# Performance work log

Measured on AMD Instinct MI355X. Metric: run time of the kernel, lower is better.

Reference implementation:

```python
import jax, jax.numpy as jnp
import numpy as np

TOP_K = 1000  # init kwarg top_k

def setup_inputs() -> dict:
    key = jax.random.key(0)
    k1, k2 = jax.random.split(key)
    scores = jax.random.uniform(k1, (8, 120000, 80), dtype=jnp.float32)
    boxes = jax.random.normal(k2, (8, 120000, 4), dtype=jnp.float32)
    return {"scores": scores, "boxes": boxes}

def reference(scores, boxes):
    # scores: [B, A, C], boxes: [B, A, 4]  (filter_per_class=True path)
    B, A, C = scores.shape
    K = min(TOP_K, A)
    # per-class top-k over anchors
    s_t = jnp.transpose(scores, (0, 2, 1))            # [B, C, A]
    vals, idx = jax.lax.top_k(s_t, K)                 # [B, C, K]
    vals = jnp.transpose(vals, (0, 2, 1))             # [B, K, C]
    idx = jnp.transpose(idx, (0, 2, 1))               # [B, K, C]
    # gather boxes along anchor dim with batch_dims=1 semantics
    b = jnp.arange(B)[:, None, None]                  # [B,1,1]
    boxes_out = boxes[b, idx]                         # [B, K, C, 4]
    return vals, boxes_out
```

## Files before the change

### kernel.cpp

```cpp
#include <hip/hip_runtime.h>


constexpr int B_ = 8;
constexpr int A_ = 120000;
constexpr int C_ = 80;
constexpr int K_ = 1000;
constexpr int NT = 256;

constexpr int S_ = 240;
constexpr int ROWS = A_ / S_;
constexpr float CUT = 0.98958333f;
constexpr float XSCALE = 1048576.0f;
constexpr int CAP = 2048;
constexpr int PCAP = 16;
constexpr int SORT1 = 1024;
constexpr int SORT2 = 2048;

constexpr size_t GCNT_OFF = 0;
constexpr size_t GCNT_BYTES = (size_t)B_ * C_ * 4;
constexpr size_t GCAND_OFF = 4096;
constexpr size_t GCAND_BYTES = (size_t)B_ * C_ * CAP * 8;
constexpr size_t WS_NEED = GCAND_OFF + GCAND_BYTES;

__device__ __forceinline__ unsigned mono_key(float f) {
    unsigned bits = __float_as_uint(f);
    return (bits & 0x80000000u) ? ~bits : (bits | 0x80000000u);
}
__device__ __forceinline__ int xbin(float v) {
    int x = (int)((v - CUT) * XSCALE);
    return x < 0 ? 0 : (x > 16383 ? 16383 : x);
}

__global__ __launch_bounds__(NT)
void stage_kernel(const float* __restrict__ scores,
                  unsigned* __restrict__ gcount,
                  unsigned long long* __restrict__ gcand) {
    const int b = blockIdx.x / S_;
    const int s = blockIdx.x % S_;
    const int t = threadIdx.x;

    __shared__ unsigned long long st[C_ * PCAP];
    __shared__ unsigned cnt[C_];
    __shared__ unsigned base[C_];

    for (int i = t; i < C_; i += NT) cnt[i] = 0;
    __syncthreads();

    const float4* slab = (const float4*)(scores + ((size_t)b * A_ + (size_t)s * ROWS) * C_);
    constexpr int NVEC = ROWS * C_ / 4;
    int c0 = (4 * t) % C_;
    int a  = s * ROWS + (4 * t) / C_;
    for (int i = t; i < NVEC; i += NT) {
        float4 v = slab[i];
        const float vv[4] = {v.x, v.y, v.z, v.w};
        #pragma unroll
        for (int e = 0; e < 4; ++e) {
            if (vv[e] >= CUT) {
                const unsigned key = __float_as_uint(vv[e]) | 0x80000000u;
                const int c = c0 + e;
                const unsigned slot = atomicAdd(&cnt[c], 1u);
                const unsigned long long pk =
                    ((unsigned long long)key << 32) | (unsigned)(~(unsigned)a);
                if (slot < (unsigned)PCAP) {
                    st[c * PCAP + slot] = pk;
                } else {
                    const int bc = b * C_ + c;
                    const unsigned g = atomicAdd(&gcount[bc], 1u);
                    if (g < (unsigned)CAP) gcand[(size_t)bc * CAP + g] = pk;
                }
            }
        }
        c0 += 64;
        a += 12;
        if (c0 >= C_) { c0 -= C_; a += 1; }
    }
    __syncthreads();

    if (t < C_) {
        const unsigned nc = cnt[t] < (unsigned)PCAP ? cnt[t] : (unsigned)PCAP;
        base[t] = nc ? atomicAdd(&gcount[b * C_ + t], nc) : 0u;
    }
    __syncthreads();

    for (int i = t; i < C_ * PCAP; i += NT) {
        const int c = i / PCAP;
        const unsigned j = (unsigned)(i % PCAP);
        const unsigned nc = cnt[c] < (unsigned)PCAP ? cnt[c] : (unsigned)PCAP;
        if (j < nc) {
            const unsigned pos = base[c] + j;
            if (pos < (unsigned)CAP)
                gcand[((size_t)(b * C_ + c)) * CAP + pos] = st[i];
        }
    }
}

__global__ __launch_bounds__(NT)
void sort_emit_kernel(const float* __restrict__ scores, const float* __restrict__ boxes,
                      const unsigned* __restrict__ gcount,
                      const unsigned long long* __restrict__ gcand,
                      float* __restrict__ out) {
    const int blk = blockIdx.x;
    const int b = blk & 7;
    const int c = blk >> 3;
    const int bc = b * C_ + c;
    const int t = threadIdx.x;

    __shared__ unsigned long long buf[SORT2];
    __shared__ unsigned hist4k[4096];
    __shared__ unsigned coarse[NT];
    __shared__ unsigned s_tb, s_m, s_mhi, s_tb2, s_m2, s_cnt;
    __shared__ unsigned s_boundBin, s_boundCnt, s_aboveAdd;

    const unsigned n = gcount[bc];
    bool fast = (n >= (unsigned)K_ && n <= (unsigned)CAP);
    int ss = SORT1;
    int mode = 0;

    if (fast) {
        const unsigned long long* src = gcand + (size_t)bc * CAP;
        for (int i = t; i < 256; i += NT) hist4k[i] = 0;
        __syncthreads();
        for (unsigned i = t; i < n; i += NT) {
            const unsigned key = (unsigned)(src[i] >> 32);
            const int x = xbin(__uint_as_float(key & 0x7FFFFFFFu));
            atomicAdd(&hist4k[x >> 7], 1u);
        }
        __syncthreads();
        if (t == 0) {
            unsigned run = 0;
            int tb = 0;
            for (int i = 127; i >= 0; --i) {
                run += hist4k[i];
                if (run >= (unsigned)K_) { tb = i; break; }
            }
            s_tb = (unsigned)tb; s_m = run; s_mhi = run - hist4k[tb]; s_cnt = 0;
        }
        __syncthreads();
        const int tb = (int)s_tb;
        const unsigned m = s_m;

        if (m > (unsigned)SORT1) {
            for (unsigned i = t; i < n; i += NT) {
                const unsigned key = (unsigned)(src[i] >> 32);
                const int x = xbin(__uint_as_float(key & 0x7FFFFFFFu));
                if ((x >> 7) == tb) atomicAdd(&hist4k[128 + (x & 127)], 1u);
            }
            __syncthreads();
            if (t == 0) {
                unsigned run = s_mhi;
                int tb2 = 0;
                for (int i = 127; i >= 0; --i) {
                    run += hist4k[128 + i];
                    if (run >= (unsigned)K_) { tb2 = i; break; }
                }
                s_tb2 = (unsigned)tb2; s_m2 = run;
            }
            __syncthreads();
            if (s_m2 <= (unsigned)SORT1)      { mode = 1; ss = SORT1; }
            else if (m <= (unsigned)SORT2)    { mode = 0; ss = SORT2; }
            else                              { fast = false; }
        }

        if (fast) {
            const int tb2 = (int)s_tb2;
            const unsigned mm = (mode == 1) ? s_m2 : s_m;
            for (unsigned i = t; i < n; i += NT) {
                const unsigned long long e = src[i];
                const unsigned key = (unsigned)(e >> 32);
                const int x = xbin(__uint_as_float(key & 0x7FFFFFFFu));
                const int fb = x >> 7;
                bool take = (mode == 0) ? (fb >= tb)
                                        : (fb > tb || (fb == tb && (x & 127) >= tb2));
                if (take) buf[atomicAdd(&s_cnt, 1u)] = e;
            }
            __syncthreads();
            for (int i = (int)mm + t; i < ss; i += NT) buf[i] = 0ull;
            __syncthreads();
        }
    }

    if (!fast) {
        ss = SORT2;
        const float* sc = scores + (size_t)b * A_ * C_ + c;
        unsigned aboveCum = 0, pref = 0, T32 = 0;
        for (int lv = 0; lv < 3; ++lv) {
            const int shift = (lv == 0) ? 20 : (lv == 1) ? 8 : 0;
            const int nb = (lv == 2) ? 256 : 4096;
            for (int i = t; i < nb; i += NT) hist4k[i] = 0;
            __syncthreads();
            for (int a = t; a < A_; a += NT) {
                unsigned key = mono_key(sc[(size_t)a * C_]);
                bool ok = (lv == 0) || (lv == 1 ? ((key >> 20) == pref) : ((key >> 8) == pref));
                if (ok) atomicAdd(&hist4k[(key >> shift) & (nb - 1)], 1u);
            }
            __syncthreads();
            const int chunk = nb / NT;
            {
                unsigned ssum = 0;
                for (int i = 0; i < chunk; ++i) ssum += hist4k[t * chunk + i];
                coarse[t] = ssum;
            }
            __syncthreads();
            if (t == 0) {
                const unsigned target = K_ - aboveCum;
                unsigned run = 0;
                int cb = NT - 1;
                for (; cb > 0; --cb) { if (run + coarse[cb] >= target) break; run += coarse[cb]; }
                int bin = cb * chunk + (chunk - 1);
                for (; bin > cb * chunk; --bin) { if (run + hist4k[bin] >= target) break; run += hist4k[bin]; }
                s_boundBin = (unsigned)bin; s_boundCnt = hist4k[bin]; s_aboveAdd = run;
            }
            __syncthreads();
            const unsigned bin = s_boundBin, bcn = s_boundCnt, addAbove = s_aboveAdd;
            __syncthreads();
            aboveCum += addAbove;
            pref = (lv == 0) ? bin : (lv == 1) ? ((pref << 12) | bin) : ((pref << 8) | bin);
            if (aboveCum + bcn <= (unsigned)SORT2 || lv == 2) {
                T32 = (lv == 0) ? (pref << 20) : (lv == 1) ? (pref << 8) : pref;
                break;
            }
        }
        if (t == 0) s_cnt = 0;
        __syncthreads();
        for (int a = t; a < A_; a += NT) {
            unsigned key = mono_key(sc[(size_t)a * C_]);
            if (key >= T32) {
                unsigned slot = atomicAdd(&s_cnt, 1u);
                if (slot < (unsigned)SORT2)
                    buf[slot] = ((unsigned long long)key << 32) | (unsigned)(~(unsigned)a);
            }
        }
        __syncthreads();
        const unsigned nn = (s_cnt < (unsigned)SORT2) ? s_cnt : (unsigned)SORT2;
        for (int i = (int)nn + t; i < SORT2; i += NT) buf[i] = 0ull;
        __syncthreads();
    }

    for (unsigned kk = 2; kk <= (unsigned)ss; kk <<= 1) {
        for (unsigned j = kk >> 1; j > 0; j >>= 1) {
            __syncthreads();
            for (int i = t; i < ss; i += NT) {
                const int ixj = i ^ (int)j;
                if (ixj > i) {
                    const bool up = ((i & kk) == 0);
                    unsigned long long x = buf[i], y = buf[ixj];
                    if ((x < y) == up) { buf[i] = y; buf[ixj] = x; }
                }
            }
        }
    }
    __syncthreads();

    float* vals_out = out;
    float* boxes_out = out + (size_t)B_ * K_ * C_;
    const float4* bx = (const float4*)(boxes + (size_t)b * A_ * 4);
    for (int kk = t; kk < K_; kk += NT) {
        const unsigned long long e = buf[kk];
        const unsigned key = (unsigned)(e >> 32);
        const unsigned aidx = ~(unsigned)e;
        const unsigned bitsv = (key & 0x80000000u) ? (key ^ 0x80000000u) : ~key;
        vals_out[((size_t)b * K_ + kk) * C_ + c] = __uint_as_float(bitsv);
        const float4 bb = bx[aidx];
        *(float4*)&boxes_out[(((size_t)b * K_ + kk) * C_ + c) * 4] = bb;
    }
}

__global__ __launch_bounds__(NT)
void topk_select_kernel(const float* __restrict__ scores,
                        const float* __restrict__ boxes,
                        float* __restrict__ out) {
    const int blk = blockIdx.x;
    const int b = blk / C_;
    const int c = blk % C_;
    const float* sc = scores + (size_t)b * A_ * C_ + c;
    constexpr int LCAP = 2048;
    __shared__ unsigned hist[4096];
    __shared__ unsigned coarse[NT];
    __shared__ unsigned long long cand[LCAP];
    __shared__ unsigned s_n, s_boundBin, s_boundCnt, s_aboveAdd;
    const int t = threadIdx.x;
    unsigned aboveCum = 0, pref = 0, T32 = 0;
    for (int lv = 0; lv < 3; ++lv) {
        const int shift = (lv == 0) ? 20 : (lv == 1) ? 8 : 0;
        const int nb = (lv == 2) ? 256 : 4096;
        for (int i = t; i < nb; i += NT) hist[i] = 0;
        __syncthreads();
        for (int a = t; a < A_; a += NT) {
            unsigned key = mono_key(sc[(size_t)a * C_]);
            bool ok = (lv == 0) || (lv == 1 ? ((key >> 20) == pref) : ((key >> 8) == pref));
            if (ok) atomicAdd(&hist[(key >> shift) & (nb - 1)], 1u);
        }
        __syncthreads();
        const int chunk = nb / NT;
        {
            unsigned ssum = 0;
            for (int i = 0; i < chunk; ++i) ssum += hist[t * chunk + i];
            coarse[t] = ssum;
        }
        __syncthreads();
        if (t == 0) {
            const unsigned target = K_ - aboveCum;
            unsigned run = 0;
            int cb = NT - 1;
            for (; cb > 0; --cb) { if (run + coarse[cb] >= target) break; run += coarse[cb]; }
            int bin = cb * chunk + (chunk - 1);
            for (; bin > cb * chunk; --bin) { if (run + hist[bin] >= target) break; run += hist[bin]; }
            s_boundBin = (unsigned)bin; s_boundCnt = hist[bin]; s_aboveAdd = run;
        }
        __syncthreads();
        const unsigned bin = s_boundBin, bcn = s_boundCnt, addAbove = s_aboveAdd;
        __syncthreads();
        aboveCum += addAbove;
        pref = (lv == 0) ? bin : (lv == 1) ? ((pref << 12) | bin) : ((pref << 8) | bin);
        if (aboveCum + bcn <= (unsigned)LCAP || lv == 2) {
            T32 = (lv == 0) ? (pref << 20) : (lv == 1) ? (pref << 8) : pref;
            break;
        }
    }
    if (t == 0) s_n = 0;
    __syncthreads();
    for (int a = t; a < A_; a += NT) {
        unsigned key = mono_key(sc[(size_t)a * C_]);
        if (key >= T32) {
            unsigned slot = atomicAdd(&s_n, 1u);
            if (slot < (unsigned)LCAP)
                cand[slot] = ((unsigned long long)key << 32) | (unsigned)(~(unsigned)a);
        }
    }
    __syncthreads();
    const unsigned n = (s_n < (unsigned)LCAP) ? s_n : (unsigned)LCAP;
    for (int i = (int)n + t; i < LCAP; i += NT) cand[i] = 0ull;
    __syncthreads();
    for (unsigned kk = 2; kk <= (unsigned)LCAP; kk <<= 1) {
        for (unsigned j = kk >> 1; j > 0; j >>= 1) {
            __syncthreads();
            for (int i = t; i < LCAP; i += NT) {
                const int ixj = i ^ (int)j;
                if (ixj > i) {
                    const bool up = ((i & kk) == 0);
                    unsigned long long x = cand[i], y = cand[ixj];
                    if ((x < y) == up) { cand[i] = y; cand[ixj] = x; }
                }
            }
        }
    }
    __syncthreads();
    float* vals_out = out;
    float* boxes_out = out + (size_t)B_ * K_ * C_;
    const float4* bx = (const float4*)(boxes + (size_t)b * A_ * 4);
    for (int kk = t; kk < K_; kk += NT) {
        const unsigned long long e = cand[kk];
        const unsigned key = (unsigned)(e >> 32);
        const unsigned aidx = ~(unsigned)e;
        const unsigned bitsv = (key & 0x80000000u) ? (key ^ 0x80000000u) : ~key;
        vals_out[((size_t)b * K_ + kk) * C_ + c] = __uint_as_float(bitsv);
        const float4 bb = bx[aidx];
        *(float4*)&boxes_out[(((size_t)b * K_ + kk) * C_ + c) * 4] = bb;
    }
}

extern "C" void kernel_launch(void* const* d_in, const int* in_sizes, int n_in,
                              void* d_out, int out_size, void* d_ws, size_t ws_size,
                              hipStream_t stream) {
    const float* scores = (const float*)d_in[0];
    const float* boxes  = (const float*)d_in[1];
    float* out = (float*)d_out;

    if (ws_size < WS_NEED) {
        hipLaunchKernelGGL(topk_select_kernel, dim3(B_ * C_), dim3(NT), 0, stream,
                           scores, boxes, out);
        return;
    }

    char* ws = (char*)d_ws;
    unsigned* gcount = (unsigned*)(ws + GCNT_OFF);
    unsigned long long* gcand = (unsigned long long*)(ws + GCAND_OFF);

    hipMemsetAsync(gcount, 0, GCNT_BYTES, stream);
    hipLaunchKernelGGL(stage_kernel, dim3(B_ * S_), dim3(NT), 0, stream,
                       scores, gcount, gcand);
    hipLaunchKernelGGL(sort_emit_kernel, dim3(B_ * C_), dim3(NT), 0, stream,
                       scores, boxes, gcount, gcand, out);
}
```

Before: 124.5 us.

## Double the sort block size, parallelize histogram threshold scans, prefetch stage loads

The sort/emit kernel now runs 512 threads per block instead of 256, so more threads share the bitonic sort and candidate passes. The single-thread serial scans that find the threshold bins are replaced by parallel suffix-sum scans over 128 bins. The stage kernel software-prefetches the next float4 of scores before processing the current one to overlap load latency with compare/atomic work. The gains come at the cost of more barriers in the scan, higher register and LDS pressure, and possibly fewer resident blocks per CU.

```diff
diff --git a/kernel.cpp b/kernel.cpp
--- a/kernel.cpp
+++ b/kernel.cpp
@@ -6,6 +6,7 @@
 constexpr int C_ = 80;
 constexpr int K_ = 1000;
 constexpr int NT = 256;
+constexpr int NT2 = 512;
 
 constexpr int S_ = 240;
 constexpr int ROWS = A_ / S_;
@@ -50,8 +51,13 @@
     constexpr int NVEC = ROWS * C_ / 4;
     int c0 = (4 * t) % C_;
     int a  = s * ROWS + (4 * t) / C_;
-    for (int i = t; i < NVEC; i += NT) {
-        float4 v = slab[i];
+    int i = t;
+    float4 v = make_float4(0.f, 0.f, 0.f, 0.f);
+    if (i < NVEC) v = slab[i];
+    while (i < NVEC) {
+        const int in = i + NT;
+        float4 vn = v;
+        if (in < NVEC) vn = slab[in];
         const float vv[4] = {v.x, v.y, v.z, v.w};
         #pragma unroll
         for (int e = 0; e < 4; ++e) {
@@ -73,6 +79,8 @@
         c0 += 64;
         a += 12;
         if (c0 >= C_) { c0 -= C_; a += 1; }
+        i = in;
+        v = vn;
     }
     __syncthreads();
 
@@ -82,19 +90,19 @@
     }
     __syncthreads();
 
-    for (int i = t; i < C_ * PCAP; i += NT) {
-        const int c = i / PCAP;
-        const unsigned j = (unsigned)(i % PCAP);
+    for (int i2 = t; i2 < C_ * PCAP; i2 += NT) {
+        const int c = i2 / PCAP;
+        const unsigned j = (unsigned)(i2 % PCAP);
         const unsigned nc = cnt[c] < (unsigned)PCAP ? cnt[c] : (unsigned)PCAP;
         if (j < nc) {
             const unsigned pos = base[c] + j;
             if (pos < (unsigned)CAP)
-                gcand[((size_t)(b * C_ + c)) * CAP + pos] = st[i];
-        }
-    }
-}
-
-__global__ __launch_bounds__(NT)
+                gcand[((size_t)(b * C_ + c)) * CAP + pos] = st[i2];
+        }
+    }
+}
+
+__global__ __launch_bounds__(NT2)
 void sort_emit_kernel(const float* __restrict__ scores, const float* __restrict__ boxes,
                       const unsigned* __restrict__ gcount,
                       const unsigned long long* __restrict__ gcand,
@@ -107,7 +115,7 @@
 
     __shared__ unsigned long long buf[SORT2];
     __shared__ unsigned hist4k[4096];
-    __shared__ unsigned coarse[NT];
+    __shared__ unsigned coarse[NT2];
     __shared__ unsigned s_tb, s_m, s_mhi, s_tb2, s_m2, s_cnt;
     __shared__ unsigned s_boundBin, s_boundCnt, s_aboveAdd;
 
@@ -118,42 +126,53 @@
 
     if (fast) {
         const unsigned long long* src = gcand + (size_t)bc * CAP;
-        for (int i = t; i < 256; i += NT) hist4k[i] = 0;
-        __syncthreads();
-        for (unsigned i = t; i < n; i += NT) {
+        for (int i = t; i < 256; i += NT2) hist4k[i] = 0;
+        __syncthreads();
+        for (unsigned i = t; i < n; i += NT2) {
             const unsigned key = (unsigned)(src[i] >> 32);
             const int x = xbin(__uint_as_float(key & 0x7FFFFFFFu));
             atomicAdd(&hist4k[x >> 7], 1u);
         }
         __syncthreads();
-        if (t == 0) {
-            unsigned run = 0;
-            int tb = 0;
-            for (int i = 127; i >= 0; --i) {
-                run += hist4k[i];
-                if (run >= (unsigned)K_) { tb = i; break; }
-            }
-            s_tb = (unsigned)tb; s_m = run; s_mhi = run - hist4k[tb]; s_cnt = 0;
-        }
+        for (int d = 1; d < 128; d <<= 1) {
+            unsigned add = 0;
+            if (t < 128 && t + d < 128) add = hist4k[t + d];
+            __syncthreads();
+            if (t < 128) hist4k[t] += add;
+            __syncthreads();
+        }
+        if (t < 128) {
+            const unsigned si = hist4k[t];
+            const unsigned snext = (t < 127) ? hist4k[t + 1] : 0u;
+            if (si >= (unsigned)K_ && snext < (unsigned)K_) {
+                s_tb = (unsigned)t; s_m = si; s_mhi = snext;
+            }
+        }
+        if (t == 0) s_cnt = 0;
         __syncthreads();
         const int tb = (int)s_tb;
         const unsigned m = s_m;
 
         if (m > (unsigned)SORT1) {
-            for (unsigned i = t; i < n; i += NT) {
+            for (unsigned i = t; i < n; i += NT2) {
                 const unsigned key = (unsigned)(src[i] >> 32);
                 const int x = xbin(__uint_as_float(key & 0x7FFFFFFFu));
                 if ((x >> 7) == tb) atomicAdd(&hist4k[128 + (x & 127)], 1u);
             }
             __syncthreads();
-            if (t == 0) {
-                unsigned run = s_mhi;
-                int tb2 = 0;
-                for (int i = 127; i >= 0; --i) {
-                    run += hist4k[128 + i];
-                    if (run >= (unsigned)K_) { tb2 = i; break; }
+            for (int d = 1; d < 128; d <<= 1) {
+                unsigned add = 0;
+                if (t < 128 && t + d < 128) add = hist4k[128 + t + d];
+                __syncthreads();
+                if (t < 128) hist4k[128 + t] += add;
+                __syncthreads();
+            }
+            if (t < 128) {
+                const unsigned si = s_mhi + hist4k[128 + t];
+                const unsigned snext = s_mhi + ((t < 127) ? hist4k[128 + t + 1] : 0u);
+                if (si >= (unsigned)K_ && snext < (unsigned)K_) {
+                    s_tb2 = (unsigned)t; s_m2 = si;
                 }
-                s_tb2 = (unsigned)tb2; s_m2 = run;
             }
             __syncthreads();
             if (s_m2 <= (unsigned)SORT1)      { mode = 1; ss = SORT1; }
@@ -164,7 +183,7 @@
         if (fast) {
             const int tb2 = (int)s_tb2;
             const unsigned mm = (mode == 1) ? s_m2 : s_m;
-            for (unsigned i = t; i < n; i += NT) {
+            for (unsigned i = t; i < n; i += NT2) {
                 const unsigned long long e = src[i];
                 const unsigned key = (unsigned)(e >> 32);
                 const int x = xbin(__uint_as_float(key & 0x7FFFFFFFu));
@@ -174,7 +193,7 @@
                 if (take) buf[atomicAdd(&s_cnt, 1u)] = e;
             }
             __syncthreads();
-            for (int i = (int)mm + t; i < ss; i += NT) buf[i] = 0ull;
+            for (int i = (int)mm + t; i < ss; i += NT2) buf[i] = 0ull;
             __syncthreads();
         }
     }
@@ -186,16 +205,17 @@
         for (int lv = 0; lv < 3; ++lv) {
             const int shift = (lv == 0) ? 20 : (lv == 1) ? 8 : 0;
             const int nb = (lv == 2) ? 256 : 4096;
-            for (int i = t; i < nb; i += NT) hist4k[i] = 0;
-            __syncthreads();
-            for (int a = t; a < A_; a += NT) {
+            for (int i = t; i < nb; i += NT2) hist4k[i] = 0;
+            __syncthreads();
+            for (int a = t; a < A_; a += NT2) {
                 unsigned key = mono_key(sc[(size_t)a * C_]);
                 bool ok = (lv == 0) || (lv == 1 ? ((key >> 20) == pref) : ((key >> 8) == pref));
                 if (ok) atomicAdd(&hist4k[(key >> shift) & (nb - 1)], 1u);
             }
             __syncthreads();
-            const int chunk = nb / NT;
-            {
+            const int active = (nb < NT2) ? nb : NT2;
+            const int chunk = nb / active;
+            if (t < active) {
                 unsigned ssum = 0;
                 for (int i = 0; i < chunk; ++i) ssum += hist4k[t * chunk + i];
                 coarse[t] = ssum;
@@ -204,7 +224,7 @@
             if (t == 0) {
                 const unsigned target = K_ - aboveCum;
                 unsigned run = 0;
-                int cb = NT - 1;
+                int cb = active - 1;
                 for (; cb > 0; --cb) { if (run + coarse[cb] >= target) break; run += coarse[cb]; }
                 int bin = cb * chunk + (chunk - 1);
                 for (; bin > cb * chunk; --bin) { if (run + hist4k[bin] >= target) break; run += hist4k[bin]; }
@@ -222,7 +242,7 @@
         }
         if (t == 0) s_cnt = 0;
         __syncthreads();
-        for (int a = t; a < A_; a += NT) {
+        for (int a = t; a < A_; a += NT2) {
             unsigned key = mono_key(sc[(size_t)a * C_]);
             if (key >= T32) {
                 unsigned slot = atomicAdd(&s_cnt, 1u);
@@ -232,14 +252,14 @@
         }
         __syncthreads();
         const unsigned nn = (s_cnt < (unsigned)SORT2) ? s_cnt : (unsigned)SORT2;
-        for (int i = (int)nn + t; i < SORT2; i += NT) buf[i] = 0ull;
+        for (int i = (int)nn + t; i < SORT2; i += NT2) buf[i] = 0ull;
         __syncthreads();
     }
 
     for (unsigned kk = 2; kk <= (unsigned)ss; kk <<= 1) {
         for (unsigned j = kk >> 1; j > 0; j >>= 1) {
             __syncthreads();
-            for (int i = t; i < ss; i += NT) {
+            for (int i = t; i < ss; i += NT2) {
                 const int ixj = i ^ (int)j;
                 if (ixj > i) {
                     const bool up = ((i & kk) == 0);
@@ -254,7 +274,7 @@
     float* vals_out = out;
     float* boxes_out = out + (size_t)B_ * K_ * C_;
     const float4* bx = (const float4*)(boxes + (size_t)b * A_ * 4);
-    for (int kk = t; kk < K_; kk += NT) {
+    for (int kk = t; kk < K_; kk += NT2) {
         const unsigned long long e = buf[kk];
         const unsigned key = (unsigned)(e >> 32);
         const unsigned aidx = ~(unsigned)e;
@@ -379,6 +399,6 @@
     hipMemsetAsync(gcount, 0, GCNT_BYTES, stream);
     hipLaunchKernelGGL(stage_kernel, dim3(B_ * S_), dim3(NT), 0, stream,
                        scores, gcount, gcand);
-    hipLaunchKernelGGL(sort_emit_kernel, dim3(B_ * C_), dim3(NT), 0, stream,
+    hipLaunchKernelGGL(sort_emit_kernel, dim3(B_ * C_), dim3(NT2), 0, stream,
                        scores, boxes, gcount, gcand, out);
 }
```

After: 103.2 us. -17.1%, faster.
